# Performance work log

Hardware: AMD Instinct MI355X
Metric: run time of the kernel (lower is better)

Reference implementation:

```python
import jax, jax.numpy as jnp
import numpy as np

B, S, DM, H, NSYN = 4, 2048, 768, 12, 4
HD = DM // H  # 64
EPS = 1e-12
SCALE = float(DM / H) ** -0.5  # 1/sqrt(head_dim)


def setup_inputs() -> dict:
    key = jax.random.key(0)
    ks = jax.random.split(key, 16)
    p = 0.02
    return {
        "hidden_states": jax.random.normal(ks[0], (B, S, DM), jnp.float32),
        "attention_mask": jnp.zeros((B, 1, 1, S), jnp.float32),
        "addi_key": jax.random.normal(ks[1], (B, NSYN, S, HD), jnp.float32),
        "addi_value": jax.random.normal(ks[2], (B, NSYN, S, HD), jnp.float32),
        "Wq": jax.random.normal(ks[3], (DM, DM), jnp.float32) * p,
        "bq": jnp.zeros((DM,), jnp.float32),
        "Wk": jax.random.normal(ks[4], (DM, DM), jnp.float32) * p,
        "bk": jnp.zeros((DM,), jnp.float32),
        "Wv": jax.random.normal(ks[5], (DM, DM), jnp.float32) * p,
        "bv": jnp.zeros((DM,), jnp.float32),
        "Wo": jax.random.normal(ks[6], (DM, DM), jnp.float32) * p,
        "bo": jnp.zeros((DM,), jnp.float32),
        "ln_g": jnp.ones((DM,), jnp.float32),
        "ln_b": jnp.zeros((DM,), jnp.float32),
    }


def _heads(x):
    # [B,S,DM] -> [B,H,S,HD]
    return x.reshape(B, S, H, HD).transpose(0, 2, 1, 3)


def reference(hidden_states, attention_mask, addi_key, addi_value,
              Wq, bq, Wk, bk, Wv, bv, Wo, bo, ln_g, ln_b):
    x = hidden_states
    q = _heads(jnp.einsum('bsi,oi->bso', x, Wq) + bq)
    k = _heads(jnp.einsum('bsi,oi->bso', x, Wk) + bk)
    v = _heads(jnp.einsum('bsi,oi->bso', x, Wv) + bv)
    # additive key/value injection on first NSYN heads
    k = k.at[:, :NSYN].add(addi_key)
    v = v.at[:, :NSYN].add(addi_value)
    scores = jnp.einsum('bhqd,bhkd->bhqk', q, k) * SCALE + attention_mask
    probs = jax.nn.softmax(scores, axis=-1)
    ctx = jnp.einsum('bhqk,bhkd->bhqd', probs, v)
    ctx = ctx.transpose(0, 2, 1, 3).reshape(B, S, DM)
    out = jnp.einsum('bsi,oi->bso', ctx, Wo) + bo
    h = out + x  # residual
    mu = jnp.mean(h, axis=-1, keepdims=True)
    var = jnp.mean((h - mu) ** 2, axis=-1, keepdims=True)
    return (h - mu) * jax.lax.rsqrt(var + EPS) * ln_g + ln_b
```

## Files before the change

kernel.cpp:

```cpp
#include <hip/hip_runtime.h>


typedef __bf16 bf16;
typedef __bf16 bf16x8 __attribute__((ext_vector_type(8)));
typedef __bf16 bf16x4 __attribute__((ext_vector_type(4)));
typedef float floatx4 __attribute__((ext_vector_type(4)));

#define BB 4
#define SS 2048
#define DM 768
#define HH 12
#define HD 64
#define NSYN 4
#define MM (BB*SS)
#define KK DM
#define SCALE 0.125f
#define LOG2E 1.4426950408889634f

#define N_X   ((size_t)MM * DM)
#define N_W   ((size_t)DM * DM)
#define N_M   ((size_t)BB * SS)

#if __has_builtin(__builtin_amdgcn_exp2f)
#define EXP2(x) __builtin_amdgcn_exp2f(x)
#else
#define EXP2(x) exp2f(x)
#endif

#define ASYNC16(gp, lp)                                                        \
    __builtin_amdgcn_global_load_lds(                                          \
        (const __attribute__((address_space(1))) unsigned int*)(gp),           \
        (__attribute__((address_space(3))) unsigned int*)(lp), 16, 0, 0)

__global__ __launch_bounds__(256) void cvt_kernel(
    const float* __restrict__ x,
    const float* __restrict__ Wq, const float* __restrict__ Wk,
    const float* __restrict__ Wv, const float* __restrict__ Wo,
    const float* __restrict__ mask,
    bf16* __restrict__ xb,
    bf16* __restrict__ Wqb, bf16* __restrict__ Wkb,
    bf16* __restrict__ Wvb, bf16* __restrict__ Wob,
    float* __restrict__ ml2e)
{
    const size_t nx4 = N_X / 4, nw4 = N_W / 4, nm4 = N_M / 4;
    size_t i = (size_t)blockIdx.x * blockDim.x + threadIdx.x;
    if (i >= nx4 + 4 * nw4) {
        size_t off = i - nx4 - 4 * nw4;
        if (off < nm4) {
            float4 m = *(const float4*)(mask + off * 4);
            float4 o = { m.x * LOG2E, m.y * LOG2E, m.z * LOG2E, m.w * LOG2E };
            *(float4*)(ml2e + off * 4) = o;
        }
        return;
    }
    const float* src; bf16* dst; size_t off;
    if (i < nx4)                { src = x;  dst = xb;  off = i; }
    else if (i < nx4 + nw4)     { src = Wq; dst = Wqb; off = i - nx4; }
    else if (i < nx4 + 2*nw4)   { src = Wk; dst = Wkb; off = i - nx4 - nw4; }
    else if (i < nx4 + 3*nw4)   { src = Wv; dst = Wvb; off = i - nx4 - 2*nw4; }
    else                        { src = Wo; dst = Wob; off = i - nx4 - 3*nw4; }
    float4 v = *(const float4*)(src + off * 4);
    bf16x4 o = { (bf16)v.x, (bf16)v.y, (bf16)v.z, (bf16)v.w };
    *(bf16x4*)(dst + off * 4) = o;
}

template<int ORD>
__device__ __forceinline__ void gemm_mainloop64(
    const bf16* __restrict__ A, const bf16* __restrict__ Bw,
    int tileM, int tileN, bf16* As, bf16* Bs, floatx4 acc[2][4])
{
    const int tid  = threadIdx.x;
    const int lane = tid & 63;
    const int wave = tid >> 6;
    const int l15 = lane & 15, quad = lane >> 4;

    const int r0a = wave * 32 + (lane >> 2);
    const int r0b = wave * 16 + (lane >> 2);
    const int cl  = (lane & 3) ^ ((lane >> 2) & 3);
    const bf16* gA = A  + (size_t)(tileM * 128 + r0a) * KK + cl * 8;
    const bf16* gB = Bw + (size_t)(tileN *  64 + r0b) * KK + cl * 8;
    bf16* lA = As + (wave * 32) * 32;
    bf16* lB = Bs + (wave * 16) * 32;

    ASYNC16(gA,           lA);
    ASYNC16(gA + 16 * KK, lA + 16 * 32);
    ASYNC16(gB,           lB);
    __syncthreads();

    const int fpc = quad ^ (l15 & 3);
    for (int kt = 0; kt < KK / 32; ++kt) {
        const int cur = kt & 1;
        if (kt + 1 < KK / 32) {
            const int nbA = (1 - cur) * 4096;
            const int nbB = (1 - cur) * 2048;
            ASYNC16(gA + (kt + 1) * 32,           lA + nbA);
            ASYNC16(gA + (kt + 1) * 32 + 16 * KK, lA + nbA + 16 * 32);
            ASYNC16(gB + (kt + 1) * 32,           lB + nbB);
        }
        const bf16* cA = As + cur * 4096;
        const bf16* cB = Bs + cur * 2048;
        bf16x8 af[2], bfr[4];
        #pragma unroll
        for (int i = 0; i < 2; ++i)
            af[i] = *(const bf16x8*)(cA + (wave * 32 + i * 16 + l15) * 32 + fpc * 8);
        #pragma unroll
        for (int j = 0; j < 4; ++j)
            bfr[j] = *(const bf16x8*)(cB + (j * 16 + l15) * 32 + fpc * 8);
        #pragma unroll
        for (int i = 0; i < 2; ++i)
            #pragma unroll
            for (int j = 0; j < 4; ++j)
                acc[i][j] = (ORD == 0)
                    ? __builtin_amdgcn_mfma_f32_16x16x32_bf16(af[i], bfr[j], acc[i][j], 0, 0, 0)
                    : __builtin_amdgcn_mfma_f32_16x16x32_bf16(bfr[j], af[i], acc[i][j], 0, 0, 0);
        __syncthreads();
    }
}

__global__ __launch_bounds__(256) void qkv_kernel(
    const bf16* __restrict__ xb,
    const bf16* __restrict__ Wqb, const float* __restrict__ bq,
    const bf16* __restrict__ Wkb, const float* __restrict__ bk,
    const bf16* __restrict__ Wvb, const float* __restrict__ bv,
    const float* __restrict__ addi_key, const float* __restrict__ addi_value,
    bf16* __restrict__ qbuf, bf16* __restrict__ kbuf, bf16* __restrict__ vtbuf)
{
    __shared__ __align__(16) bf16 As[2 * 128 * 32];
    __shared__ __align__(16) bf16 Bs[2 * 64 * 32];
    const int u = blockIdx.x;
    const int tileM = u & 63;
    const int r     = u >> 6;
    const int tileN = r % 12;
    const int z     = r / 12;
    const bf16* W     = (z == 0) ? Wqb : (z == 1) ? Wkb : Wvb;
    const float* bias = (z == 0) ? bq  : (z == 1) ? bk  : bv;

    floatx4 acc[2][4];
    #pragma unroll
    for (int i = 0; i < 2; ++i)
        #pragma unroll
        for (int j = 0; j < 4; ++j) { floatx4 zv = {0.f, 0.f, 0.f, 0.f}; acc[i][j] = zv; }

    const int lane = threadIdx.x & 63, wave = threadIdx.x >> 6;
    const int l15 = lane & 15, quad = lane >> 4;

    if (z == 2) {
        gemm_mainloop64<0>(xb, W, tileM, tileN, As, Bs, acc);
        #pragma unroll
        for (int i = 0; i < 2; ++i) {
            const int sg0 = tileM * 128 + wave * 32 + i * 16 + quad * 4;
            const int b = sg0 >> 11, s0 = sg0 & 2047;
            #pragma unroll
            for (int j = 0; j < 4; ++j) {
                const int o = tileN * 64 + j * 16 + l15;
                const float bv_ = bias[o];
                const int h = o >> 6, d = o & 63;
                float vv[4];
                #pragma unroll
                for (int rr = 0; rr < 4; ++rr) {
                    vv[rr] = acc[i][j][rr] + bv_;
                    if (h < NSYN)
                        vv[rr] += addi_value[(((size_t)b * NSYN + h) * SS + s0 + rr) * HD + d];
                }
                bf16x4 pk = { (bf16)vv[0], (bf16)vv[1], (bf16)vv[2], (bf16)vv[3] };
                *(bf16x4*)(vtbuf + (((size_t)b * HH + h) * HD + d) * SS + s0) = pk;
            }
        }
    } else {
        gemm_mainloop64<1>(xb, W, tileM, tileN, As, Bs, acc);
        #pragma unroll
        for (int i = 0; i < 2; ++i) {
            const int sg = tileM * 128 + wave * 32 + i * 16 + l15;
            const int b = sg >> 11, s = sg & 2047;
            #pragma unroll
            for (int j = 0; j < 4; ++j) {
                const int o0 = tileN * 64 + j * 16 + quad * 4;
                const int h = o0 >> 6, d0 = o0 & 63;
                float4 b4 = *(const float4*)(bias + o0);
                float vv[4] = { acc[i][j][0] + b4.x, acc[i][j][1] + b4.y,
                                acc[i][j][2] + b4.z, acc[i][j][3] + b4.w };
                if (z == 1 && h < NSYN) {
                    float4 a4 = *(const float4*)(addi_key +
                        (((size_t)b * NSYN + h) * SS + s) * HD + d0);
                    vv[0] += a4.x; vv[1] += a4.y; vv[2] += a4.z; vv[3] += a4.w;
                }
                if (z == 0) {
                    bf16x4 pk = { (bf16)(vv[0] * SCALE), (bf16)(vv[1] * SCALE),
                                  (bf16)(vv[2] * SCALE), (bf16)(vv[3] * SCALE) };
                    *(bf16x4*)(qbuf + (((size_t)b * HH + h) * SS + s) * HD + d0) = pk;
                } else {
                    bf16x4 pk = { (bf16)vv[0], (bf16)vv[1], (bf16)vv[2], (bf16)vv[3] };
                    *(bf16x4*)(kbuf + (((size_t)b * HH + h) * SS + s) * HD + d0) = pk;
                }
            }
        }
    }
}

__global__ __launch_bounds__(256, 3) void attn_kernel(
    const bf16* __restrict__ qbuf, const bf16* __restrict__ kbuf,
    const bf16* __restrict__ vtbuf, const float* __restrict__ ml2e,
    bf16* __restrict__ ctx)
{
    __shared__ __align__(16) bf16 Ks[2 * 64 * 64];
    __shared__ __align__(16) bf16 Vt[2 * 64 * 64];
    __shared__ __align__(16) bf16 Ps[4][32 * 72];

    const int u  = blockIdx.x;
    const int bh = u % 48;
    const int qt = u / 48;
    const int b  = bh / 12;
    const int h  = bh % 12;
    const size_t bhs = ((size_t)b * HH + h) * SS * HD;
    const int tid = threadIdx.x, lane = tid & 63, wave = tid >> 6;
    const int l15 = lane & 15, quad = lane >> 4;
    const int q0 = qt * 128 + wave * 32;

    const int sr  = wave * 16 + (lane >> 3);
    const int scl = (lane & 7) ^ ((lane >> 3) & 7);
    const bf16* gK = kbuf  + bhs + (size_t)sr * HD + scl * 8;
    const bf16* gV = vtbuf + bhs + (size_t)sr * SS + scl * 8;
    bf16* lK = Ks + (wave * 16) * 64;
    bf16* lV = Vt + (wave * 16) * 64;

    bf16x8 qf[2][2];
    #pragma unroll
    for (int n = 0; n < 2; ++n)
        #pragma unroll
        for (int c = 0; c < 2; ++c)
            qf[n][c] = *(const bf16x8*)(qbuf + bhs +
                (size_t)(q0 + n * 16 + l15) * HD + c * 32 + quad * 8);

    floatx4 acco[2][4];
    #pragma unroll
    for (int n = 0; n < 2; ++n)
        #pragma unroll
        for (int t = 0; t < 4; ++t) { floatx4 zv = {0.f, 0.f, 0.f, 0.f}; acco[n][t] = zv; }
    float lrun[2] = { 0.f, 0.f };

    const float* mb = ml2e + (size_t)b * SS;
    bf16* Pw = Ps[wave];

    #pragma unroll
    for (int p = 0; p < 2; ++p) {
        ASYNC16(gK + (size_t)p * 8 * HD,  lK + p * 512);
        ASYNC16(gV + (size_t)p * 8 * SS,  lV + p * 512);
    }
    __syncthreads();

    for (int kt = 0; kt < SS / 64; ++kt) {
        const int cur = kt & 1;
        if (kt + 1 < SS / 64) {
            const int nb = (1 - cur) * 4096;
            #pragma unroll
            for (int p = 0; p < 2; ++p) {
                ASYNC16(gK + ((size_t)(kt + 1) * 64 + p * 8) * HD, lK + nb + p * 512);
                ASYNC16(gV + (size_t)p * 8 * SS + (kt + 1) * 64,   lV + nb + p * 512);
            }
        }
        const bf16* cK = Ks + cur * 4096;
        const bf16* cV = Vt + cur * 4096;

        floatx4 sacc[2][4];
        #pragma unroll
        for (int n = 0; n < 2; ++n)
            #pragma unroll
            for (int j = 0; j < 4; ++j) { floatx4 zv = {0.f, 0.f, 0.f, 0.f}; sacc[n][j] = zv; }
        #pragma unroll
        for (int c = 0; c < 2; ++c) {
            const int pc = (4 * c + quad) ^ (l15 & 7);
            #pragma unroll
            for (int j = 0; j < 4; ++j) {
                bf16x8 af = *(const bf16x8*)(cK + (j * 16 + l15) * 64 + pc * 8);
                #pragma unroll
                for (int n = 0; n < 2; ++n)
                    sacc[n][j] = __builtin_amdgcn_mfma_f32_16x16x32_bf16(af, qf[n][c], sacc[n][j], 0, 0, 0);
            }
        }

        #pragma unroll
        for (int j = 0; j < 4; ++j) {
            float4 mk = *(const float4*)(mb + kt * 64 + j * 16 + quad * 4);
            #pragma unroll
            for (int n = 0; n < 2; ++n) {
                float p0 = EXP2(__builtin_fmaf(sacc[n][j][0], LOG2E, mk.x));
                float p1 = EXP2(__builtin_fmaf(sacc[n][j][1], LOG2E, mk.y));
                float p2 = EXP2(__builtin_fmaf(sacc[n][j][2], LOG2E, mk.z));
                float p3 = EXP2(__builtin_fmaf(sacc[n][j][3], LOG2E, mk.w));
                lrun[n] += (p0 + p1) + (p2 + p3);
                bf16x4 pk = { (bf16)p0, (bf16)p1, (bf16)p2, (bf16)p3 };
                *(bf16x4*)(Pw + (n * 16 + l15) * 72 + j * 16 + quad * 4) = pk;
            }
        }

        #pragma unroll
        for (int c = 0; c < 2; ++c) {
            const int pc = (4 * c + quad) ^ (l15 & 7);
            bf16x8 pfr[2];
            #pragma unroll
            for (int n = 0; n < 2; ++n)
                pfr[n] = *(const bf16x8*)(Pw + (n * 16 + l15) * 72 + c * 32 + quad * 8);
            #pragma unroll
            for (int t = 0; t < 4; ++t) {
                bf16x8 af = *(const bf16x8*)(cV + (t * 16 + l15) * 64 + pc * 8);
                #pragma unroll
                for (int n = 0; n < 2; ++n)
                    acco[n][t] = __builtin_amdgcn_mfma_f32_16x16x32_bf16(af, pfr[n], acco[n][t], 0, 0, 0);
            }
        }
        __syncthreads();
    }

    #pragma unroll
    for (int n = 0; n < 2; ++n) {
        lrun[n] += __shfl_xor(lrun[n], 16);
        lrun[n] += __shfl_xor(lrun[n], 32);
    }

    #pragma unroll
    for (int n = 0; n < 2; ++n) {
        const float inv = 1.0f / lrun[n];
        bf16* crow = ctx + ((size_t)(b * SS + q0 + n * 16 + l15)) * DM + h * HD;
        #pragma unroll
        for (int t = 0; t < 4; ++t) {
            bf16x4 ov = { (bf16)(acco[n][t][0] * inv), (bf16)(acco[n][t][1] * inv),
                          (bf16)(acco[n][t][2] * inv), (bf16)(acco[n][t][3] * inv) };
            *(bf16x4*)(crow + t * 16 + quad * 4) = ov;
        }
    }
}

__global__ __launch_bounds__(256) void oproj_kernel(
    const bf16* __restrict__ ctx, const bf16* __restrict__ Wob,
    const float* __restrict__ bo, const float* __restrict__ x,
    bf16* __restrict__ hbuf)
{
    __shared__ __align__(16) bf16 As[2 * 128 * 32];
    __shared__ __align__(16) bf16 Bs[2 * 64 * 32];
    const int u = blockIdx.x;
    const int tileM = u & 63;
    const int tileN = u >> 6;

    floatx4 acc[2][4];
    #pragma unroll
    for (int i = 0; i < 2; ++i)
        #pragma unroll
        for (int j = 0; j < 4; ++j) { floatx4 zv = {0.f, 0.f, 0.f, 0.f}; acc[i][j] = zv; }

    gemm_mainloop64<1>(ctx, Wob, tileM, tileN, As, Bs, acc);

    const int lane = threadIdx.x & 63, wave = threadIdx.x >> 6;
    const int l15 = lane & 15, quad = lane >> 4;
    #pragma unroll
    for (int i = 0; i < 2; ++i) {
        const int sg = tileM * 128 + wave * 32 + i * 16 + l15;
        #pragma unroll
        for (int j = 0; j < 4; ++j) {
            const int o0 = tileN * 64 + j * 16 + quad * 4;
            float4 b4 = *(const float4*)(bo + o0);
            float4 r4 = *(const float4*)(x + (size_t)sg * DM + o0);
            bf16x4 pk = { (bf16)(acc[i][j][0] + b4.x + r4.x),
                          (bf16)(acc[i][j][1] + b4.y + r4.y),
                          (bf16)(acc[i][j][2] + b4.z + r4.z),
                          (bf16)(acc[i][j][3] + b4.w + r4.w) };
            *(bf16x4*)(hbuf + (size_t)sg * DM + o0) = pk;
        }
    }
}

__global__ __launch_bounds__(256) void ln_kernel(
    const bf16* __restrict__ hbuf, const float* __restrict__ g,
    const float* __restrict__ be, float* __restrict__ out)
{
    const int row  = blockIdx.x * 4 + (threadIdx.x >> 6);
    const int lane = threadIdx.x & 63;
    const bf16* hr = hbuf + (size_t)row * DM;

    bf16x8 va = *(const bf16x8*)(hr + lane * 8);
    bf16x4 vb = *(const bf16x4*)(hr + 512 + lane * 4);
    float v[12];
    #pragma unroll
    for (int i = 0; i < 8; ++i) v[i] = (float)va[i];
    #pragma unroll
    for (int i = 0; i < 4; ++i) v[8 + i] = (float)vb[i];

    float s = 0.f;
    #pragma unroll
    for (int i = 0; i < 12; ++i) s += v[i];
    #pragma unroll
    for (int m = 1; m < 64; m <<= 1) s += __shfl_xor(s, m);
    const float mu = s * (1.0f / DM);

    float s2 = 0.f;
    #pragma unroll
    for (int i = 0; i < 12; ++i) { v[i] -= mu; s2 += v[i] * v[i]; }
    #pragma unroll
    for (int m = 1; m < 64; m <<= 1) s2 += __shfl_xor(s2, m);
    const float rsv = rsqrtf(s2 * (1.0f / DM) + 1e-12f);

    float* orow = out + (size_t)row * DM;
    const int c0 = lane * 8, c1 = 512 + lane * 4;
    float4 g0 = *(const float4*)(g + c0),     g1 = *(const float4*)(g + c0 + 4);
    float4 g2 = *(const float4*)(g + c1);
    float4 b0 = *(const float4*)(be + c0),    b1 = *(const float4*)(be + c0 + 4);
    float4 b2 = *(const float4*)(be + c1);
    float4 o0 = { v[0]*rsv*g0.x + b0.x, v[1]*rsv*g0.y + b0.y,
                  v[2]*rsv*g0.z + b0.z, v[3]*rsv*g0.w + b0.w };
    float4 o1 = { v[4]*rsv*g1.x + b1.x, v[5]*rsv*g1.y + b1.y,
                  v[6]*rsv*g1.z + b1.z, v[7]*rsv*g1.w + b1.w };
    float4 o2 = { v[8]*rsv*g2.x + b2.x, v[9]*rsv*g2.y + b2.y,
                  v[10]*rsv*g2.z + b2.z, v[11]*rsv*g2.w + b2.w };
    *(float4*)(orow + c0)     = o0;
    *(float4*)(orow + c0 + 4) = o1;
    *(float4*)(orow + c1)     = o2;
}

extern "C" void kernel_launch(void* const* d_in, const int* in_sizes, int n_in,
                              void* d_out, int out_size, void* d_ws, size_t ws_size,
                              hipStream_t stream)
{
    const float* x    = (const float*)d_in[0];
    const float* mask = (const float*)d_in[1];
    const float* akey = (const float*)d_in[2];
    const float* aval = (const float*)d_in[3];
    const float* Wq = (const float*)d_in[4];  const float* bq = (const float*)d_in[5];
    const float* Wk = (const float*)d_in[6];  const float* bk = (const float*)d_in[7];
    const float* Wv = (const float*)d_in[8];  const float* bv = (const float*)d_in[9];
    const float* Wo = (const float*)d_in[10]; const float* bo = (const float*)d_in[11];
    const float* lng = (const float*)d_in[12]; const float* lnb = (const float*)d_in[13];
    float* outp = (float*)d_out;

    const size_t nqkv = (size_t)BB * HH * SS * HD;
    char* ws = (char*)d_ws;
    bf16*  xb   = (bf16*)ws;   ws += N_X  * sizeof(bf16);
    bf16*  Wqb  = (bf16*)ws;   ws += N_W  * sizeof(bf16);
    bf16*  Wkb  = (bf16*)ws;   ws += N_W  * sizeof(bf16);
    bf16*  Wvb  = (bf16*)ws;   ws += N_W  * sizeof(bf16);
    bf16*  Wob  = (bf16*)ws;   ws += N_W  * sizeof(bf16);
    float* ml2e = (float*)ws;  ws += N_M  * sizeof(float);
    bf16*  qbuf = (bf16*)ws;   ws += nqkv * sizeof(bf16);
    bf16*  kbuf = (bf16*)ws;   ws += nqkv * sizeof(bf16);
    bf16*  vtbuf= (bf16*)ws;   ws += nqkv * sizeof(bf16);
    bf16*  ctxb = (bf16*)ws;   ws += nqkv * sizeof(bf16);
    bf16*  hbuf = (bf16*)ws;   ws += nqkv * sizeof(bf16);

    const size_t ncvt = (N_X + 4 * N_W + N_M) / 4;
    const int cvt_blocks = (int)((ncvt + 255) / 256);
    cvt_kernel<<<cvt_blocks, 256, 0, stream>>>(x, Wq, Wk, Wv, Wo, mask,
                                               xb, Wqb, Wkb, Wvb, Wob, ml2e);

    qkv_kernel<<<2304, 256, 0, stream>>>(xb, Wqb, bq, Wkb, bk, Wvb, bv, akey, aval,
                                         qbuf, kbuf, vtbuf);
    attn_kernel<<<768, 256, 0, stream>>>(qbuf, kbuf, vtbuf, ml2e, ctxb);
    oproj_kernel<<<768, 256, 0, stream>>>(ctxb, Wob, bo, x, hbuf);
    ln_kernel<<<MM / 4, 256, 0, stream>>>(hbuf, lng, lnb, outp);
}
```

Measured before the change: 275.9 us.

## Keep attention probabilities in registers via permlane swaps, halve per-wave query rows

The attention kernel no longer stages the softmax probability tile through shared memory. It repacks the score-MFMA output layout into the PV-MFMA operand layout in registers using permlane32/permlane16 swap instructions. Each wave now handles 16 query rows instead of 32, so the grid doubles to 1536 blocks and the occupancy hint rises to 5. The aim is to remove the LDS write/read round trip for P and improve occupancy. The cost is that each K/V tile loaded into LDS is reused by half as many queries, which doubles total K/V traffic. The register permute also depends on the lane mapping matching exactly.

```diff
diff --git a/kernel.cpp b/kernel.cpp
--- a/kernel.cpp
+++ b/kernel.cpp
@@ -5,6 +5,7 @@
 typedef __bf16 bf16x8 __attribute__((ext_vector_type(8)));
 typedef __bf16 bf16x4 __attribute__((ext_vector_type(4)));
 typedef float floatx4 __attribute__((ext_vector_type(4)));
+typedef unsigned int uint2v __attribute__((ext_vector_type(2)));
 
 #define BB 4
 #define SS 2048
@@ -31,6 +32,23 @@
     __builtin_amdgcn_global_load_lds(                                          \
         (const __attribute__((address_space(1))) unsigned int*)(gp),           \
         (__attribute__((address_space(3))) unsigned int*)(lp), 16, 0, 0)
+
+static __device__ __forceinline__ void pl32_swap(unsigned int& a, unsigned int& b) {
+#if __has_builtin(__builtin_amdgcn_permlane32_swap)
+    uint2v r = __builtin_amdgcn_permlane32_swap(a, b, false, false);
+    a = r[0]; b = r[1];
+#else
+    asm volatile("v_permlane32_swap_b32 %0, %1" : "+v"(a), "+v"(b));
+#endif
+}
+static __device__ __forceinline__ void pl16_swap(unsigned int& a, unsigned int& b) {
+#if __has_builtin(__builtin_amdgcn_permlane16_swap)
+    uint2v r = __builtin_amdgcn_permlane16_swap(a, b, false, false);
+    a = r[0]; b = r[1];
+#else
+    asm volatile("v_permlane16_swap_b32 %0, %1" : "+v"(a), "+v"(b));
+#endif
+}
 
 __global__ __launch_bounds__(256) void cvt_kernel(
     const float* __restrict__ x,
@@ -197,14 +215,13 @@
     }
 }
 
-__global__ __launch_bounds__(256, 3) void attn_kernel(
+__global__ __launch_bounds__(256, 5) void attn_kernel(
     const bf16* __restrict__ qbuf, const bf16* __restrict__ kbuf,
     const bf16* __restrict__ vtbuf, const float* __restrict__ ml2e,
     bf16* __restrict__ ctx)
 {
     __shared__ __align__(16) bf16 Ks[2 * 64 * 64];
     __shared__ __align__(16) bf16 Vt[2 * 64 * 64];
-    __shared__ __align__(16) bf16 Ps[4][32 * 72];
 
     const int u  = blockIdx.x;
     const int bh = u % 48;
@@ -214,7 +231,7 @@
     const size_t bhs = ((size_t)b * HH + h) * SS * HD;
     const int tid = threadIdx.x, lane = tid & 63, wave = tid >> 6;
     const int l15 = lane & 15, quad = lane >> 4;
-    const int q0 = qt * 128 + wave * 32;
+    const int q0 = qt * 64 + wave * 16;
 
     const int sr  = wave * 16 + (lane >> 3);
     const int scl = (lane & 7) ^ ((lane >> 3) & 7);
@@ -223,23 +240,18 @@
     bf16* lK = Ks + (wave * 16) * 64;
     bf16* lV = Vt + (wave * 16) * 64;
 
-    bf16x8 qf[2][2];
-    #pragma unroll
-    for (int n = 0; n < 2; ++n)
-        #pragma unroll
-        for (int c = 0; c < 2; ++c)
-            qf[n][c] = *(const bf16x8*)(qbuf + bhs +
-                (size_t)(q0 + n * 16 + l15) * HD + c * 32 + quad * 8);
-
-    floatx4 acco[2][4];
-    #pragma unroll
-    for (int n = 0; n < 2; ++n)
-        #pragma unroll
-        for (int t = 0; t < 4; ++t) { floatx4 zv = {0.f, 0.f, 0.f, 0.f}; acco[n][t] = zv; }
-    float lrun[2] = { 0.f, 0.f };
+    bf16x8 qf[2];
+    #pragma unroll
+    for (int c = 0; c < 2; ++c)
+        qf[c] = *(const bf16x8*)(qbuf + bhs +
+            (size_t)(q0 + l15) * HD + c * 32 + quad * 8);
+
+    floatx4 acco[4];
+    #pragma unroll
+    for (int t = 0; t < 4; ++t) { floatx4 zv = {0.f, 0.f, 0.f, 0.f}; acco[t] = zv; }
+    float lrun = 0.f;
 
     const float* mb = ml2e + (size_t)b * SS;
-    bf16* Pw = Ps[wave];
 
     #pragma unroll
     for (int p = 0; p < 2; ++p) {
@@ -261,72 +273,65 @@
         const bf16* cK = Ks + cur * 4096;
         const bf16* cV = Vt + cur * 4096;
 
-        floatx4 sacc[2][4];
-        #pragma unroll
-        for (int n = 0; n < 2; ++n)
-            #pragma unroll
-            for (int j = 0; j < 4; ++j) { floatx4 zv = {0.f, 0.f, 0.f, 0.f}; sacc[n][j] = zv; }
+        floatx4 sacc[4];
+        #pragma unroll
+        for (int j = 0; j < 4; ++j) { floatx4 zv = {0.f, 0.f, 0.f, 0.f}; sacc[j] = zv; }
         #pragma unroll
         for (int c = 0; c < 2; ++c) {
             const int pc = (4 * c + quad) ^ (l15 & 7);
             #pragma unroll
             for (int j = 0; j < 4; ++j) {
                 bf16x8 af = *(const bf16x8*)(cK + (j * 16 + l15) * 64 + pc * 8);
-                #pragma unroll
-                for (int n = 0; n < 2; ++n)
-                    sacc[n][j] = __builtin_amdgcn_mfma_f32_16x16x32_bf16(af, qf[n][c], sacc[n][j], 0, 0, 0);
+                sacc[j] = __builtin_amdgcn_mfma_f32_16x16x32_bf16(af, qf[c], sacc[j], 0, 0, 0);
             }
         }
 
+        unsigned int w[4][2];
         #pragma unroll
         for (int j = 0; j < 4; ++j) {
             float4 mk = *(const float4*)(mb + kt * 64 + j * 16 + quad * 4);
-            #pragma unroll
-            for (int n = 0; n < 2; ++n) {
-                float p0 = EXP2(__builtin_fmaf(sacc[n][j][0], LOG2E, mk.x));
-                float p1 = EXP2(__builtin_fmaf(sacc[n][j][1], LOG2E, mk.y));
-                float p2 = EXP2(__builtin_fmaf(sacc[n][j][2], LOG2E, mk.z));
-                float p3 = EXP2(__builtin_fmaf(sacc[n][j][3], LOG2E, mk.w));
-                lrun[n] += (p0 + p1) + (p2 + p3);
-                bf16x4 pk = { (bf16)p0, (bf16)p1, (bf16)p2, (bf16)p3 };
-                *(bf16x4*)(Pw + (n * 16 + l15) * 72 + j * 16 + quad * 4) = pk;
-            }
-        }
+            float p0 = EXP2(__builtin_fmaf(sacc[j][0], LOG2E, mk.x));
+            float p1 = EXP2(__builtin_fmaf(sacc[j][1], LOG2E, mk.y));
+            float p2 = EXP2(__builtin_fmaf(sacc[j][2], LOG2E, mk.z));
+            float p3 = EXP2(__builtin_fmaf(sacc[j][3], LOG2E, mk.w));
+            lrun += (p0 + p1) + (p2 + p3);
+            union { bf16x4 v; unsigned int u2[2]; } pk;
+            pk.v = (bf16x4){ (bf16)p0, (bf16)p1, (bf16)p2, (bf16)p3 };
+            w[j][0] = pk.u2[0];
+            w[j][1] = pk.u2[1];
+        }
+        pl32_swap(w[0][0], w[1][0]);  pl32_swap(w[0][1], w[1][1]);
+        pl32_swap(w[2][0], w[3][0]);  pl32_swap(w[2][1], w[3][1]);
+        pl16_swap(w[0][0], w[1][0]);  pl16_swap(w[0][1], w[1][1]);
+        pl16_swap(w[2][0], w[3][0]);  pl16_swap(w[2][1], w[3][1]);
+        union { unsigned int u2[4]; bf16x8 v; } pb[2];
+        pb[0].u2[0] = w[0][0]; pb[0].u2[1] = w[0][1];
+        pb[0].u2[2] = w[1][0]; pb[0].u2[3] = w[1][1];
+        pb[1].u2[0] = w[2][0]; pb[1].u2[1] = w[2][1];
+        pb[1].u2[2] = w[3][0]; pb[1].u2[3] = w[3][1];
 
         #pragma unroll
         for (int c = 0; c < 2; ++c) {
             const int pc = (4 * c + quad) ^ (l15 & 7);
-            bf16x8 pfr[2];
-            #pragma unroll
-            for (int n = 0; n < 2; ++n)
-                pfr[n] = *(const bf16x8*)(Pw + (n * 16 + l15) * 72 + c * 32 + quad * 8);
             #pragma unroll
             for (int t = 0; t < 4; ++t) {
                 bf16x8 af = *(const bf16x8*)(cV + (t * 16 + l15) * 64 + pc * 8);
-                #pragma unroll
-                for (int n = 0; n < 2; ++n)
-                    acco[n][t] = __builtin_amdgcn_mfma_f32_16x16x32_bf16(af, pfr[n], acco[n][t], 0, 0, 0);
+                acco[t] = __builtin_amdgcn_mfma_f32_16x16x32_bf16(af, pb[c].v, acco[t], 0, 0, 0);
             }
         }
         __syncthreads();
     }
 
-    #pragma unroll
-    for (int n = 0; n < 2; ++n) {
-        lrun[n] += __shfl_xor(lrun[n], 16);
-        lrun[n] += __shfl_xor(lrun[n], 32);
-    }
-
-    #pragma unroll
-    for (int n = 0; n < 2; ++n) {
-        const float inv = 1.0f / lrun[n];
-        bf16* crow = ctx + ((size_t)(b * SS + q0 + n * 16 + l15)) * DM + h * HD;
-        #pragma unroll
-        for (int t = 0; t < 4; ++t) {
-            bf16x4 ov = { (bf16)(acco[n][t][0] * inv), (bf16)(acco[n][t][1] * inv),
-                          (bf16)(acco[n][t][2] * inv), (bf16)(acco[n][t][3] * inv) };
-            *(bf16x4*)(crow + t * 16 + quad * 4) = ov;
-        }
+    lrun += __shfl_xor(lrun, 16);
+    lrun += __shfl_xor(lrun, 32);
+    const float inv = 1.0f / lrun;
+
+    bf16* crow = ctx + ((size_t)(b * SS + q0 + l15)) * DM + h * HD;
+    #pragma unroll
+    for (int t = 0; t < 4; ++t) {
+        bf16x4 ov = { (bf16)(acco[t][0] * inv), (bf16)(acco[t][1] * inv),
+                      (bf16)(acco[t][2] * inv), (bf16)(acco[t][3] * inv) };
+        *(bf16x4*)(crow + t * 16 + quad * 4) = ov;
     }
 }
 
@@ -451,7 +456,7 @@
 
     qkv_kernel<<<2304, 256, 0, stream>>>(xb, Wqb, bq, Wkb, bk, Wvb, bv, akey, aval,
                                          qbuf, kbuf, vtbuf);
-    attn_kernel<<<768, 256, 0, stream>>>(qbuf, kbuf, vtbuf, ml2e, ctxb);
+    attn_kernel<<<1536, 256, 0, stream>>>(qbuf, kbuf, vtbuf, ml2e, ctxb);
     oproj_kernel<<<768, 256, 0, stream>>>(ctxb, Wob, bo, x, hbuf);
     ln_kernel<<<MM / 4, 256, 0, stream>>>(hbuf, lng, lnb, outp);
 }
```

Measured after the change: 289.6 us. +5.0%, slower.
